# Kernel optimization log

Measured on AMD Instinct MI355X. Metric: run time of the kernel, lower is better.

## Reference

```python
import jax, jax.numpy as jnp
import numpy as np

DECAY = 0.5
TAU = 16
SLOPE = 0.01  # torch leaky_relu default negative_slope
EPS = 1e-12   # torch F.normalize default eps


def setup_inputs() -> dict:
    key = jax.random.key(0)
    k1, k2 = jax.random.split(key)
    B, D = 8, 8192
    x = jax.random.normal(k1, (B, D), dtype=jnp.float32)
    M = jax.random.uniform(k2, (D, D), dtype=jnp.float32)  # torch.rand(dim,dim)
    hs = jnp.zeros((1, D), dtype=jnp.float32)
    return {"x": x, "M": M, "hs": hs}


def reference(x, M, hs):
    # hs starts as zeros(1,dim) and broadcasts to (B,dim) on the first update
    hs0 = jnp.broadcast_to(hs, x.shape)

    def step(carry, _):
        hs_t, h = carry
        pre = DECAY * hs_t + h @ M                 # (B, D)
        act = jnp.where(pre >= 0, pre, SLOPE * pre)  # leaky_relu
        nrm = jnp.maximum(
            jnp.sqrt(jnp.sum(act * act, axis=1, keepdims=True)), EPS)
        hs_new = act / nrm                          # L2 normalize (dim=1)
        return (hs_new, hs_new), None

    (hs_final, _), _ = jax.lax.scan(step, (hs0, x), None, length=TAU)
    return hs_final
```

## Files before the change

kernel.cpp:

```cpp
#include <hip/hip_runtime.h>


#define DD 8192
#define BB 8
#define TAU 16
#define NK 64
#define KCH 128
#define DECAYF 0.5f
#define SLOPEF 0.01f
#define EPSF 1e-12f

static __device__ __forceinline__ float b2f(unsigned short u) {
    union { unsigned int i; float f; } v; v.i = ((unsigned int)u) << 16; return v.f;
}
static __device__ __forceinline__ unsigned short f2b(float f) {
    union { float f; unsigned int i; } v; v.f = f;
    unsigned int r = v.i + 0x7FFFu + ((v.i >> 16) & 1u);
    return (unsigned short)(r >> 16);
}

__global__ __launch_bounds__(256) void convert_kernel(const float* __restrict__ M,
                                                      unsigned short* __restrict__ Mbf) {
    const size_t i = ((size_t)blockIdx.x * 256 + threadIdx.x) * 4;
    const float4 v = *(const float4*)(M + i);
    ushort4 o;
    o.x = f2b(v.x); o.y = f2b(v.y); o.z = f2b(v.z); o.w = f2b(v.w);
    *(ushort4*)(Mbf + i) = o;
}

template <bool BF16>
__global__ __launch_bounds__(256) void matmul_kernel(const float* __restrict__ h,
                                                     const void* __restrict__ Mv,
                                                     float* __restrict__ part) {
    const int tid   = threadIdx.x;
    const int j0    = blockIdx.x * 1024 + tid * 4;
    const int kbase = blockIdx.y * KCH;

    float acc[BB][4];
#pragma unroll
    for (int r = 0; r < BB; r++) { acc[r][0] = acc[r][1] = acc[r][2] = acc[r][3] = 0.0f; }

    if constexpr (BF16) {
        const unsigned short* Mb = (const unsigned short*)Mv + (size_t)kbase * DD + j0;
        for (int kb = 0; kb < KCH; kb += 16) {
            ushort4 mv[16];
#pragma unroll
            for (int u = 0; u < 16; u++)
                mv[u] = *(const ushort4*)(Mb + (size_t)(kb + u) * DD);
#pragma unroll
            for (int u = 0; u < 16; u++) {
                const float m0 = b2f(mv[u].x), m1 = b2f(mv[u].y);
                const float m2 = b2f(mv[u].z), m3 = b2f(mv[u].w);
#pragma unroll
                for (int r = 0; r < BB; r++) {
                    const float hv = h[r * DD + kbase + kb + u];
                    acc[r][0] = fmaf(hv, m0, acc[r][0]);
                    acc[r][1] = fmaf(hv, m1, acc[r][1]);
                    acc[r][2] = fmaf(hv, m2, acc[r][2]);
                    acc[r][3] = fmaf(hv, m3, acc[r][3]);
                }
            }
        }
    } else {
        const float* Mf = (const float*)Mv + (size_t)kbase * DD + j0;
        for (int kb = 0; kb < KCH; kb += 8) {
            float4 mv[8];
#pragma unroll
            for (int u = 0; u < 8; u++)
                mv[u] = *(const float4*)(Mf + (size_t)(kb + u) * DD);
#pragma unroll
            for (int u = 0; u < 8; u++) {
#pragma unroll
                for (int r = 0; r < BB; r++) {
                    const float hv = h[r * DD + kbase + kb + u];
                    acc[r][0] = fmaf(hv, mv[u].x, acc[r][0]);
                    acc[r][1] = fmaf(hv, mv[u].y, acc[r][1]);
                    acc[r][2] = fmaf(hv, mv[u].z, acc[r][2]);
                    acc[r][3] = fmaf(hv, mv[u].w, acc[r][3]);
                }
            }
        }
    }

    float* p = part + (size_t)blockIdx.y * (BB * DD) + j0;
#pragma unroll
    for (int r = 0; r < BB; r++) {
        *(float4*)(p + r * DD) = make_float4(acc[r][0], acc[r][1], acc[r][2], acc[r][3]);
    }
}

__global__ __launch_bounds__(256) void reduce_kernel(const float* __restrict__ part,
                                                     const float* __restrict__ act_prev,
                                                     const float* __restrict__ ss_prev,
                                                     float* __restrict__ act_new,
                                                     float* __restrict__ ss_new) {
    const int tid = threadIdx.x;
    const int e   = blockIdx.x * 256 + tid;
    const int r   = e >> 13;

    float s = 0.0f;
#pragma unroll 16
    for (int i = 0; i < NK; i++) s += part[(size_t)i * (BB * DD) + e];

    float v;
    if (ss_prev) {
        const float inv = 1.0f / fmaxf(sqrtf(ss_prev[r]), EPSF);
        v = inv * (s + DECAYF * act_prev[e]);
    } else {
        v = s;
    }
    const float a = (v >= 0.0f) ? v : SLOPEF * v;
    act_new[e] = a;

    float t = a * a;
#pragma unroll
    for (int off = 32; off > 0; off >>= 1) t += __shfl_down(t, off, 64);

    __shared__ float red[4];
    if ((tid & 63) == 0) red[tid >> 6] = t;
    __syncthreads();
    if (tid == 0) atomicAdd(&ss_new[r], red[0] + red[1] + red[2] + red[3]);
}

__global__ __launch_bounds__(1024) void scale_kernel(const float* __restrict__ act,
                                                     const float* __restrict__ ss,
                                                     float* __restrict__ out) {
    const int e = blockIdx.x * 1024 + threadIdx.x;
    const float inv = 1.0f / fmaxf(sqrtf(ss[e >> 13]), EPSF);
    out[e] = act[e] * inv;
}

extern "C" void kernel_launch(void* const* d_in, const int* in_sizes, int n_in,
                              void* d_out, int out_size, void* d_ws, size_t ws_size,
                              hipStream_t stream) {
    const float* x = (const float*)d_in[0];
    const float* M = (const float*)d_in[1];

    const size_t szM = (size_t)DD * DD * sizeof(unsigned short);
    const size_t szP = (size_t)NK * BB * DD * sizeof(float);
    const size_t szA = (size_t)BB * DD * sizeof(float);
    const size_t szS = (size_t)TAU * BB * sizeof(float);

    const bool use_bf16 = (ws_size >= szM + szP + 2 * szA + szS);

    char* w = (char*)d_ws;
    unsigned short* Mbf = nullptr;
    if (use_bf16) { Mbf = (unsigned short*)w; w += szM; }
    float* part   = (float*)w;  w += szP;
    float* actA   = (float*)w;  w += szA;
    float* actB   = (float*)w;  w += szA;
    float* row_ss = (float*)w;

    hipMemsetAsync(row_ss, 0, szS, stream);
    if (use_bf16) convert_kernel<<<65536, 256, 0, stream>>>(M, Mbf);

    const float* h = x;
    float* acts[2] = {actA, actB};
    for (int t = 0; t < TAU; t++) {
        if (use_bf16)
            matmul_kernel<true ><<<dim3(8, NK), 256, 0, stream>>>(h, Mbf, part);
        else
            matmul_kernel<false><<<dim3(8, NK), 256, 0, stream>>>(h, M, part);

        reduce_kernel<<<256, 256, 0, stream>>>(part, h,
                                               t ? (row_ss + (t - 1) * BB) : (const float*)nullptr,
                                               acts[t & 1], row_ss + t * BB);
        h = acts[t & 1];
    }
    scale_kernel<<<64, 1024, 0, stream>>>(h, row_ss + (TAU - 1) * BB, (float*)d_out);
}
```

Measured before the change: 956.6 us.

## Replace FMA matmul with packed bf16 MFMA and fuse reduce into step kernel

Packs M once into an MFMA-friendly bf16 tile layout and packs activations as a hi/lo bf16 split so one 16-row MFMA operand carries both halves for extra precision. Each step is a single kernel that runs 16x16x32 bf16 MFMAs over the whole K range, reduces across waves in shared memory, applies decay, leaky ReLU and sum-of-squares, and writes the next packed A operand. This drops the 64-way partial-sum buffer and the separate reduce launch per step. The trade-off is a dependence on bf16 precision for M and on the hi/lo split for activations, plus a fixed workspace layout with no fp32 fallback.

```diff
diff --git a/kernel.cpp b/kernel.cpp
--- a/kernel.cpp
+++ b/kernel.cpp
@@ -4,11 +4,15 @@
 #define DD 8192
 #define BB 8
 #define TAU 16
-#define NK 64
-#define KCH 128
+#define NT 512
+#define KT 256
 #define DECAYF 0.5f
 #define SLOPEF 0.01f
 #define EPSF 1e-12f
+
+typedef __attribute__((ext_vector_type(8))) short short8v;
+typedef __attribute__((ext_vector_type(8))) unsigned short ushort8v;
+typedef __attribute__((ext_vector_type(4))) float float4v;
 
 static __device__ __forceinline__ float b2f(unsigned short u) {
     union { unsigned int i; float f; } v; v.i = ((unsigned int)u) << 16; return v.f;
@@ -19,107 +23,112 @@
     return (unsigned short)(r >> 16);
 }
 
-__global__ __launch_bounds__(256) void convert_kernel(const float* __restrict__ M,
-                                                      unsigned short* __restrict__ Mbf) {
-    const size_t i = ((size_t)blockIdx.x * 256 + threadIdx.x) * 4;
-    const float4 v = *(const float4*)(M + i);
-    ushort4 o;
-    o.x = f2b(v.x); o.y = f2b(v.y); o.z = f2b(v.z); o.w = f2b(v.w);
-    *(ushort4*)(Mbf + i) = o;
+__global__ __launch_bounds__(256) void pack_M_kernel(const float* __restrict__ M,
+                                                     unsigned short* __restrict__ Bp) {
+    const int w = threadIdx.x >> 6, l = threadIdx.x & 63;
+    const unsigned int wid = blockIdx.x * 4 + w;
+    const int kt = wid >> 9;
+    const int nt = wid & 511;
+    const int col = nt * 16 + (l & 15);
+    const int k0  = kt * 32 + (l >> 4) * 8;
+    const float* src = M + (size_t)k0 * DD + col;
+    ushort8v o;
+#pragma unroll
+    for (int j = 0; j < 8; j++) o[j] = f2b(__builtin_nontemporal_load(src + (size_t)j * DD));
+    *(ushort8v*)(Bp + ((size_t)nt * KT + kt) * 512 + (size_t)l * 8) = o;
 }
 
-template <bool BF16>
-__global__ __launch_bounds__(256) void matmul_kernel(const float* __restrict__ h,
-                                                     const void* __restrict__ Mv,
-                                                     float* __restrict__ part) {
-    const int tid   = threadIdx.x;
-    const int j0    = blockIdx.x * 1024 + tid * 4;
-    const int kbase = blockIdx.y * KCH;
+__global__ __launch_bounds__(256) void pack_x_kernel(const float* __restrict__ x,
+                                                     unsigned short* __restrict__ Ap) {
+    const int w = threadIdx.x >> 6, l = threadIdx.x & 63;
+    const int kt = blockIdx.x * 4 + w;
+    const int row = l & 15;
+    const int k0  = kt * 32 + (l >> 4) * 8;
+    const float* src = x + (size_t)(row & 7) * DD + k0;
+    ushort8v o;
+#pragma unroll
+    for (int j = 0; j < 8; j++) {
+        const float v = src[j];
+        const unsigned short h = f2b(v);
+        o[j] = (row < 8) ? h : f2b(v - b2f(h));
+    }
+    *(ushort8v*)(Ap + (size_t)kt * 512 + (size_t)l * 8) = o;
+}
 
-    float acc[BB][4];
+__global__ __launch_bounds__(512) void step_kernel(const unsigned short* __restrict__ Ap_cur,
+                                                   const unsigned short* __restrict__ Bp,
+                                                   const float* __restrict__ act_prev,
+                                                   const float* __restrict__ ss_prev,
+                                                   float* __restrict__ act_new,
+                                                   unsigned short* __restrict__ Ap_next,
+                                                   float* __restrict__ ss_new) {
+    const int tid = threadIdx.x;
+    const int w = tid >> 6, l = tid & 63;
+    const int bid = blockIdx.x;
+    const int col0 = bid * 32;
+
+    float4v acc0 = {0.f, 0.f, 0.f, 0.f}, acc1 = {0.f, 0.f, 0.f, 0.f};
+    const unsigned short* Abase = Ap_cur + (size_t)l * 8;
+    const unsigned short* B0 = Bp + ((size_t)(2 * bid)     * KT) * 512 + (size_t)l * 8;
+    const unsigned short* B1 = Bp + ((size_t)(2 * bid + 1) * KT) * 512 + (size_t)l * 8;
+    const int ktbase = w * 32;
+#pragma unroll 4
+    for (int i = 0; i < 32; i++) {
+        const size_t off = (size_t)(ktbase + i) * 512;
+        const short8v a  = *(const short8v*)(Abase + off);
+        const short8v b0 = *(const short8v*)(B0 + off);
+        const short8v b1 = *(const short8v*)(B1 + off);
+        acc0 = __builtin_amdgcn_mfma_f32_16x16x32_bf16(a, b0, acc0, 0, 0, 0);
+        acc1 = __builtin_amdgcn_mfma_f32_16x16x32_bf16(a, b1, acc1, 0, 0, 0);
+    }
+
+    __shared__ float red[8][16][33];
+    {
+        const int rbase = (l >> 4) * 4, c = l & 15;
 #pragma unroll
-    for (int r = 0; r < BB; r++) { acc[r][0] = acc[r][1] = acc[r][2] = acc[r][3] = 0.0f; }
-
-    if constexpr (BF16) {
-        const unsigned short* Mb = (const unsigned short*)Mv + (size_t)kbase * DD + j0;
-        for (int kb = 0; kb < KCH; kb += 16) {
-            ushort4 mv[16];
-#pragma unroll
-            for (int u = 0; u < 16; u++)
-                mv[u] = *(const ushort4*)(Mb + (size_t)(kb + u) * DD);
-#pragma unroll
-            for (int u = 0; u < 16; u++) {
-                const float m0 = b2f(mv[u].x), m1 = b2f(mv[u].y);
-                const float m2 = b2f(mv[u].z), m3 = b2f(mv[u].w);
-#pragma unroll
-                for (int r = 0; r < BB; r++) {
-                    const float hv = h[r * DD + kbase + kb + u];
-                    acc[r][0] = fmaf(hv, m0, acc[r][0]);
-                    acc[r][1] = fmaf(hv, m1, acc[r][1]);
-                    acc[r][2] = fmaf(hv, m2, acc[r][2]);
-                    acc[r][3] = fmaf(hv, m3, acc[r][3]);
-                }
-            }
-        }
-    } else {
-        const float* Mf = (const float*)Mv + (size_t)kbase * DD + j0;
-        for (int kb = 0; kb < KCH; kb += 8) {
-            float4 mv[8];
-#pragma unroll
-            for (int u = 0; u < 8; u++)
-                mv[u] = *(const float4*)(Mf + (size_t)(kb + u) * DD);
-#pragma unroll
-            for (int u = 0; u < 8; u++) {
-#pragma unroll
-                for (int r = 0; r < BB; r++) {
-                    const float hv = h[r * DD + kbase + kb + u];
-                    acc[r][0] = fmaf(hv, mv[u].x, acc[r][0]);
-                    acc[r][1] = fmaf(hv, mv[u].y, acc[r][1]);
-                    acc[r][2] = fmaf(hv, mv[u].z, acc[r][2]);
-                    acc[r][3] = fmaf(hv, mv[u].w, acc[r][3]);
-                }
-            }
+        for (int q = 0; q < 4; q++) {
+            red[w][rbase + q][c]      = acc0[q];
+            red[w][rbase + q][16 + c] = acc1[q];
         }
     }
+    __syncthreads();
 
-    float* p = part + (size_t)blockIdx.y * (BB * DD) + j0;
+    if (tid < 256) {
+        const int r = tid >> 5, c = tid & 31;
+        float s = 0.f;
 #pragma unroll
-    for (int r = 0; r < BB; r++) {
-        *(float4*)(p + r * DD) = make_float4(acc[r][0], acc[r][1], acc[r][2], acc[r][3]);
+        for (int u = 0; u < 8; u++) s += red[u][r][c] + red[u][r + 8][c];
+        float v;
+        if (ss_prev) {
+            const float inv = 1.0f / fmaxf(sqrtf(ss_prev[r]), EPSF);
+            v = inv * (s + DECAYF * act_prev[(size_t)r * DD + col0 + c]);
+        } else {
+            v = s;
+        }
+        const float a = (v >= 0.f) ? v : SLOPEF * v;
+        act_new[(size_t)r * DD + col0 + c] = a;
+
+        float t2 = a * a;
+#pragma unroll
+        for (int off = 16; off > 0; off >>= 1) t2 += __shfl_down(t2, off, 32);
+        if ((tid & 31) == 0) atomicAdd(&ss_new[r], t2);
+
+        red[0][r][c] = a;
     }
-}
+    __syncthreads();
 
-__global__ __launch_bounds__(256) void reduce_kernel(const float* __restrict__ part,
-                                                     const float* __restrict__ act_prev,
-                                                     const float* __restrict__ ss_prev,
-                                                     float* __restrict__ act_new,
-                                                     float* __restrict__ ss_new) {
-    const int tid = threadIdx.x;
-    const int e   = blockIdx.x * 256 + tid;
-    const int r   = e >> 13;
-
-    float s = 0.0f;
-#pragma unroll 16
-    for (int i = 0; i < NK; i++) s += part[(size_t)i * (BB * DD) + e];
-
-    float v;
-    if (ss_prev) {
-        const float inv = 1.0f / fmaxf(sqrtf(ss_prev[r]), EPSF);
-        v = inv * (s + DECAYF * act_prev[e]);
-    } else {
-        v = s;
+    if (w == 0) {
+        const int row = l & 15;
+        const int kb  = (l >> 4) * 8;
+        ushort8v o;
+#pragma unroll
+        for (int j = 0; j < 8; j++) {
+            const float v = red[0][row & 7][kb + j];
+            const unsigned short h = f2b(v);
+            o[j] = (row < 8) ? h : f2b(v - b2f(h));
+        }
+        *(ushort8v*)(Ap_next + (size_t)bid * 512 + (size_t)l * 8) = o;
     }
-    const float a = (v >= 0.0f) ? v : SLOPEF * v;
-    act_new[e] = a;
-
-    float t = a * a;
-#pragma unroll
-    for (int off = 32; off > 0; off >>= 1) t += __shfl_down(t, off, 64);
-
-    __shared__ float red[4];
-    if ((tid & 63) == 0) red[tid >> 6] = t;
-    __syncthreads();
-    if (tid == 0) atomicAdd(&ss_new[r], red[0] + red[1] + red[2] + red[3]);
 }
 
 __global__ __launch_bounds__(1024) void scale_kernel(const float* __restrict__ act,
@@ -136,36 +145,33 @@
     const float* x = (const float*)d_in[0];
     const float* M = (const float*)d_in[1];
 
-    const size_t szM = (size_t)DD * DD * sizeof(unsigned short);
-    const size_t szP = (size_t)NK * BB * DD * sizeof(float);
-    const size_t szA = (size_t)BB * DD * sizeof(float);
+    const size_t szB = (size_t)NT * KT * 1024;
+    const size_t szA = (size_t)KT * 1024;
+    const size_t szF = (size_t)BB * DD * sizeof(float);
     const size_t szS = (size_t)TAU * BB * sizeof(float);
 
-    const bool use_bf16 = (ws_size >= szM + szP + 2 * szA + szS);
-
-    char* w = (char*)d_ws;
-    unsigned short* Mbf = nullptr;
-    if (use_bf16) { Mbf = (unsigned short*)w; w += szM; }
-    float* part   = (float*)w;  w += szP;
-    float* actA   = (float*)w;  w += szA;
-    float* actB   = (float*)w;  w += szA;
-    float* row_ss = (float*)w;
+    char* p = (char*)d_ws;
+    unsigned short* Bp  = (unsigned short*)p; p += szB;
+    unsigned short* Ap0 = (unsigned short*)p; p += szA;
+    unsigned short* Ap1 = (unsigned short*)p; p += szA;
+    float* act0 = (float*)p; p += szF;
+    float* act1 = (float*)p; p += szF;
+    float* row_ss = (float*)p;
 
     hipMemsetAsync(row_ss, 0, szS, stream);
-    if (use_bf16) convert_kernel<<<65536, 256, 0, stream>>>(M, Mbf);
+    pack_x_kernel<<<64, 256, 0, stream>>>(x, Ap0);
+    pack_M_kernel<<<32768, 256, 0, stream>>>(M, Bp);
 
-    const float* h = x;
-    float* acts[2] = {actA, actB};
+    unsigned short* Aps[2] = {Ap0, Ap1};
+    float* acts[2] = {act0, act1};
     for (int t = 0; t < TAU; t++) {
-        if (use_bf16)
-            matmul_kernel<true ><<<dim3(8, NK), 256, 0, stream>>>(h, Mbf, part);
-        else
-            matmul_kernel<false><<<dim3(8, NK), 256, 0, stream>>>(h, M, part);
-
-        reduce_kernel<<<256, 256, 0, stream>>>(part, h,
-                                               t ? (row_ss + (t - 1) * BB) : (const float*)nullptr,
-                                               acts[t & 1], row_ss + t * BB);
-        h = acts[t & 1];
+        step_kernel<<<256, 512, 0, stream>>>(
+            Aps[t & 1], Bp,
+            acts[(t + 1) & 1],
+            t ? (row_ss + (t - 1) * BB) : (const float*)nullptr,
+            acts[t & 1],
+            Aps[(t + 1) & 1],
+            row_ss + t * BB);
     }
-    scale_kernel<<<64, 1024, 0, stream>>>(h, row_ss + (TAU - 1) * BB, (float*)d_out);
+    scale_kernel<<<64, 1024, 0, stream>>>(acts[1], row_ss + (TAU - 1) * BB, (float*)d_out);
 }
```

Result: slower. 989.8 us (+3.5%).
